# Kernel tuning notes

Hardware: AMD Instinct MI355X
Metric: run time of the kernel (lower is better)

Reference implementation:

```python
import jax, jax.numpy as jnp
import numpy as np

B, T, C, H = 2, 512, 1024, 16
D = C // H          # head dim 64
CS = 64             # chunk_size
NS_STEPS = 5
OMEGA_W = 8
KCONV = 4

# Polar Express per-iteration quintic coefficients (Amsel et al. 2025)
_PE_COEFFS = [
    (8.28721201814563, -23.595886519098837, 17.300387312530933),
    (4.107059111542203, -2.9478499167379106, 0.5448431082926601),
    (3.9486908534822946, -2.908902115962949, 0.5518191394370137),
    (3.3184196573706015, -2.488488024314874, 0.51004894012372),
    (2.300652019954817, -1.6689039845747493, 0.4188073119525673),
    (1.891301407787398, -1.2679958271945868, 0.37680408948524835),
    (1.8750014808534479, -1.2500016453999487, 0.3750001645474248),
    (1.875, -1.25, 0.375),
]

def _polar_express(X):
    # X: (..., D, D). Normalize to spectral-norm <= 1 via Frobenius bound, then iterate.
    nrm = jnp.sqrt(jnp.sum(X * X, axis=(-2, -1), keepdims=True)) + 1e-7
    Xn = X / (nrm * 1.01)
    for a, b, c in _PE_COEFFS[:NS_STEPS]:
        A = Xn @ jnp.swapaxes(Xn, -1, -2)
        Xn = a * Xn + (b * A + c * (A @ A)) @ Xn
    return Xn

def _polar_express_ste(X):
    # straight-through: forward = PE(X), backward = identity
    return X + jax.lax.stop_gradient(_polar_express(X) - X)

def _rms_norm(x):
    return x * jax.lax.rsqrt(jnp.mean(x * x, axis=-1, keepdims=True) + 1e-6)

def _poly_features(x):
    # phi(x) = sum_{i=1..p} x^i / i!  with poly_degree=2
    return x + 0.5 * x * x

def _short_conv(x, w, b):
    # causal depthwise conv; x:(B,T,C), w:(C,1,K), b:(C,)
    xc = jnp.transpose(x, (0, 2, 1))
    xc = jnp.pad(xc, ((0, 0), (0, 0), (KCONV - 1, 0)))
    y = jax.lax.conv_general_dilated(
        xc, w, window_strides=(1,), padding="VALID",
        dimension_numbers=("NCW", "OIW", "NCW"), feature_group_count=x.shape[-1])
    y = y + b[:, None]
    return jnp.transpose(y, (0, 2, 1))

def _linear_scan(h_init, gates, inputs):
    # h_t = g_t * h_{t-1} + in_t ; gates (B,cs,H), inputs (B,cs,H,D,D)
    g = gates[..., None, None]
    first = g[:, :1] * h_init[:, None] + inputs[:, :1]
    mod_in = jnp.concatenate([first, inputs[:, 1:]], axis=1)
    mod_g = jnp.concatenate([jnp.zeros_like(g[:, :1]), g[:, 1:]], axis=1)
    def comb(a, b):
        ga, xa = a; gb, xb = b
        return (ga * gb, gb * xa + xb)
    _, h_all = jax.lax.associative_scan(comb, (mod_g, mod_in), axis=1)
    return h_all, h_all[:, -1]

def _omega_aggregate(u, gamma):
    # sliding-window sum of gamma_i * u_i over last OMEGA_W positions, via cumsum
    cs = u.shape[1]
    cum = jnp.cumsum(gamma * u, axis=1)
    if OMEGA_W >= cs:
        return cum
    shifted = jnp.concatenate([jnp.zeros_like(cum[:, :OMEGA_W]), cum[:, :-OMEGA_W]], axis=1)
    return cum - shifted


def setup_inputs() -> dict:
    key = jax.random.key(0)
    ks = jax.random.split(key, 16)
    s = 0.02
    return {
        "x":   jax.random.normal(ks[0], (B, T, C), jnp.float32),
        "Wq":  jax.random.normal(ks[1], (C, C), jnp.float32) * s,
        "Wk":  jax.random.normal(ks[2], (C, C), jnp.float32) * s,
        "Wv":  jax.random.normal(ks[3], (C, C), jnp.float32) * s,
        "Wo":  jax.random.normal(ks[4], (C, C), jnp.float32) * s,
        "cqw": jax.random.normal(ks[5], (C, 1, KCONV), jnp.float32) * s,
        "cqb": jnp.zeros((C,), jnp.float32),
        "ckw": jax.random.normal(ks[6], (C, 1, KCONV), jnp.float32) * s,
        "ckb": jnp.zeros((C,), jnp.float32),
        "cvw": jax.random.normal(ks[7], (C, 1, KCONV), jnp.float32) * s,
        "cvb": jnp.zeros((C,), jnp.float32),
        "Wa":  jax.random.normal(ks[8], (H, C), jnp.float32) * s,
        "We":  jax.random.normal(ks[9], (H, C), jnp.float32) * s,
        "Wt":  jax.random.normal(ks[10], (H, C), jnp.float32) * s,
        "Wg":  jax.random.normal(ks[11], (H, C), jnp.float32) * s,
    }


def reference(x, Wq, Wk, Wv, Wo, cqw, cqb, ckw, ckb, cvw, cvb, Wa, We, Wt, Wg):
    Bsz, Tlen, Cdim = x.shape
    q = _short_conv(x @ Wq.T, cqw, cqb).reshape(Bsz, Tlen, H, D)
    k = _short_conv(x @ Wk.T, ckw, ckb).reshape(Bsz, Tlen, H, D)
    v = _short_conv(x @ Wv.T, cvw, cvb).reshape(Bsz, Tlen, H, D)
    q = _poly_features(_rms_norm(q))
    k = _poly_features(_rms_norm(k))
    alpha = jax.nn.sigmoid(x @ Wa.T)   # (B,T,H) memory retention gate
    eta   = jax.nn.sigmoid(x @ We.T)   # learning rate gate
    theta = jax.nn.sigmoid(x @ Wt.T)   # momentum gate
    gamma = jax.nn.sigmoid(x @ Wg.T)   # omega context gate

    nC = Tlen // CS
    def chunked(a):  # (B,T,...) -> (nC,B,CS,...)
        return jnp.moveaxis(a.reshape(Bsz, nC, CS, *a.shape[2:]), 1, 0)
    qc, kc, vc = chunked(q), chunked(k), chunked(v)
    ac, ec, tc, gc = chunked(alpha), chunked(eta), chunked(theta), chunked(gamma)

    M0 = jnp.zeros((Bsz, H, D, D), x.dtype)
    S0 = jnp.zeros((Bsz, H, D, D), x.dtype)

    def step(carry, inp):
        M, S = carry
        q_c, k_c, v_c, a_c, e_c, t_c, g_c = inp
        pred = jnp.einsum("bhvk,bchk->bchv", M, k_c)
        err = pred - v_c
        u = 2.0 * jnp.einsum("bchv,bchk->bchvk", err, k_c)     # per-token gradient
        u = _omega_aggregate(u, g_c[..., None, None])           # omega window
        mom_in = -(e_c[..., None, None] * u)
        chunk_S, S = _linear_scan(S, t_c, mom_in)               # momentum scan
        chunk_S_orth = _polar_express_ste(chunk_S)              # orthogonalize
        M_all, M = _linear_scan(M, a_c, chunk_S_orth)           # memory scan
        y_c = jnp.einsum("bchvk,bchk->bchv", M_all, q_c)        # read memory
        return (M, S), y_c

    _, ys = jax.lax.scan(step, (M0, S0), (qc, kc, vc, ac, ec, tc, gc))
    y = jnp.moveaxis(ys, 0, 1).reshape(Bsz, Tlen, H, D)
    y = _rms_norm(y).reshape(Bsz, Tlen, Cdim)
    return y @ Wo.T
```

## Files before the change

kernel.cpp:

```cpp
#include <hip/hip_runtime.h>

constexpr int Bsz = 2, Tsz = 512, Csz = 1024, Hsz = 16, Dsz = 64, CSz = 64;
constexpr int NCHUNK = 8, OW = 8;

typedef __attribute__((ext_vector_type(8))) _Float16 half8;
typedef __attribute__((ext_vector_type(4))) _Float16 half4;
typedef __attribute__((ext_vector_type(16))) float f32x16;

constexpr float INV_S = 1.0f / 2048.0f;

__device__ __forceinline__ void split_f16(float v, _Float16& hi, _Float16& lo) {
  _Float16 h = (_Float16)v;
  float r = v - (float)h;
  hi = h;
  lo = (_Float16)(r * 2048.0f);
}

#define MFMA2(accH, accL, ah, al, bh, bl)                                     \
  accH = __builtin_amdgcn_mfma_f32_32x32x16_f16(ah, bh, accH, 0, 0, 0);       \
  accL = __builtin_amdgcn_mfma_f32_32x32x16_f16(ah, bl, accL, 0, 0, 0);       \
  accL = __builtin_amdgcn_mfma_f32_32x32x16_f16(al, bh, accL, 0, 0, 0);

__global__ __launch_bounds__(256) void split_all_kernel(
    const float* __restrict__ x, const float* __restrict__ Wq,
    const float* __restrict__ Wk, const float* __restrict__ Wv,
    const float* __restrict__ Wo, const float* __restrict__ Wa,
    const float* __restrict__ We, const float* __restrict__ Wt,
    const float* __restrict__ Wg,
    _Float16* __restrict__ xh, _Float16* __restrict__ xl,
    _Float16* __restrict__ Wqh, _Float16* __restrict__ Wql,
    _Float16* __restrict__ Wkh, _Float16* __restrict__ Wkl,
    _Float16* __restrict__ Wvh, _Float16* __restrict__ Wvl,
    _Float16* __restrict__ Woh, _Float16* __restrict__ Wol,
    _Float16* __restrict__ gWh, _Float16* __restrict__ gWl) {
  const int y = blockIdx.y;
  const int tid = threadIdx.x;
  if (y < 5) {
    const float* src = (y == 0 ? x : y == 1 ? Wq : y == 2 ? Wk : y == 3 ? Wv : Wo);
    _Float16* dh = (y == 0 ? xh : y == 1 ? Wqh : y == 2 ? Wkh : y == 3 ? Wvh : Woh);
    _Float16* dl = (y == 0 ? xl : y == 1 ? Wql : y == 2 ? Wkl : y == 3 ? Wvl : Wol);
    size_t i = ((size_t)blockIdx.x * 256 + tid) * 4;
    float4 v = *(const float4*)(src + i);
    half4 h, l;
#pragma unroll
    for (int j = 0; j < 4; ++j) { _Float16 hh, ll; split_f16((&v.x)[j], hh, ll); h[j] = hh; l[j] = ll; }
    *(half4*)(dh + i) = h;
    *(half4*)(dl + i) = l;
  } else {
    if (blockIdx.x >= 64) return;
    size_t i = ((size_t)blockIdx.x * 256 + tid) * 4;
    int gsel = (int)(i >> 14);
    int off = (int)(i & 16383);
    const float* src = (gsel == 0 ? Wa : gsel == 1 ? We : gsel == 2 ? Wt : Wg);
    float4 v = *(const float4*)(src + off);
    half4 h, l;
#pragma unroll
    for (int j = 0; j < 4; ++j) { _Float16 hh, ll; split_f16((&v.x)[j], hh, ll); h[j] = hh; l[j] = ll; }
    *(half4*)(gWh + i) = h;
    *(half4*)(gWl + i) = l;
  }
}

__device__ __forceinline__ void gemm64_core(const _Float16* __restrict__ Agh,
                                            const _Float16* __restrict__ Agl,
                                            const _Float16* __restrict__ Bgh,
                                            const _Float16* __restrict__ Bgl,
                                            int m0, int n0, int tid, char* LB,
                                            f32x16& accH, f32x16& accL) {
  const int lane = tid & 63, wv = tid >> 6;
  const int mb = (wv >> 1) << 5, nb = (wv & 1) << 5;
  const int lr = tid >> 2;
  const int lch = (tid & 3) << 4;
  const int cb = lch << 1;
  const int wb0 = (lr << 7) + (cb ^ ((lr & 7) << 4));
  const int wb1 = (lr << 7) + ((cb + 16) ^ ((lr & 7) << 4));
  const _Float16* pah = Agh + (size_t)(m0 + lr) * Csz + lch;
  const _Float16* pal = Agl + (size_t)(m0 + lr) * Csz + lch;
  const _Float16* pbh = Bgh + (size_t)(n0 + lr) * Csz + lch;
  const _Float16* pbl = Bgl + (size_t)(n0 + lr) * Csz + lch;
  int ra_m[4], ra_n[4];
#pragma unroll
  for (int ks = 0; ks < 4; ++ks) {
    int rm = mb + (lane & 31), rn = nb + (lane & 31);
    int cB = (ks << 5) + ((lane >> 5) << 4);
    ra_m[ks] = (rm << 7) + (cB ^ ((rm & 7) << 4));
    ra_n[ks] = (rn << 7) + (cB ^ ((rn & 7) << 4));
  }
#pragma unroll
  for (int r = 0; r < 16; ++r) { accH[r] = 0.f; accL[r] = 0.f; }
  for (int k0 = 0; k0 < Csz; k0 += 64) {
    half8 vah0 = *(const half8*)(pah + k0), vah1 = *(const half8*)(pah + k0 + 8);
    half8 val0 = *(const half8*)(pal + k0), val1 = *(const half8*)(pal + k0 + 8);
    half8 vbh0 = *(const half8*)(pbh + k0), vbh1 = *(const half8*)(pbh + k0 + 8);
    half8 vbl0 = *(const half8*)(pbl + k0), vbl1 = *(const half8*)(pbl + k0 + 8);
    __syncthreads();
    *(half8*)(LB + wb0) = vah0;          *(half8*)(LB + wb1) = vah1;
    *(half8*)(LB + 8192 + wb0) = val0;   *(half8*)(LB + 8192 + wb1) = val1;
    *(half8*)(LB + 16384 + wb0) = vbh0;  *(half8*)(LB + 16384 + wb1) = vbh1;
    *(half8*)(LB + 24576 + wb0) = vbl0;  *(half8*)(LB + 24576 + wb1) = vbl1;
    __syncthreads();
    __builtin_amdgcn_s_setprio(1);
#pragma unroll
    for (int ks = 0; ks < 4; ++ks) {
      half8 ah = *(const half8*)(LB + ra_m[ks]);
      half8 al = *(const half8*)(LB + 8192 + ra_m[ks]);
      half8 bh = *(const half8*)(LB + 16384 + ra_n[ks]);
      half8 bl = *(const half8*)(LB + 24576 + ra_n[ks]);
      MFMA2(accH, accL, ah, al, bh, bl);
    }
    __builtin_amdgcn_s_setprio(0);
  }
}

__global__ __launch_bounds__(256) void qkvg_mfma(
    const _Float16* __restrict__ xh, const _Float16* __restrict__ xl,
    const _Float16* __restrict__ Wqh, const _Float16* __restrict__ Wql,
    const _Float16* __restrict__ Wkh, const _Float16* __restrict__ Wkl,
    const _Float16* __restrict__ Wvh, const _Float16* __restrict__ Wvl,
    const _Float16* __restrict__ gWh, const _Float16* __restrict__ gWl,
    float* __restrict__ qlin, float* __restrict__ klin, float* __restrict__ vlin,
    float* __restrict__ ga, float* __restrict__ ge,
    float* __restrict__ gt, float* __restrict__ gg) {
  __shared__ __attribute__((aligned(16))) char LB[32768];
  const int tid = threadIdx.x;
  const int by = blockIdx.y;
  const int m0 = blockIdx.x << 6;
  const _Float16 *Bh, *Bl;
  int n0;
  if (by < 48) {
    const int mat = by >> 4;
    n0 = (by & 15) << 6;
    Bh = (mat == 0 ? Wqh : mat == 1 ? Wkh : Wvh);
    Bl = (mat == 0 ? Wql : mat == 1 ? Wkl : Wvl);
  } else {
    n0 = 0;
    Bh = gWh;
    Bl = gWl;
  }
  f32x16 accH, accL;
  gemm64_core(xh, xl, Bh, Bl, m0, n0, tid, LB, accH, accL);
  const int lane = tid & 63, wv = tid >> 6;
  const int mb = (wv >> 1) << 5, nb = (wv & 1) << 5;
  const int crow = (lane >> 5) << 2, ccol = lane & 31;
  if (by < 48) {
    const int mat = by >> 4;
    float* O = (mat == 0 ? qlin : mat == 1 ? klin : vlin);
#pragma unroll
    for (int r = 0; r < 16; ++r) {
      int row = mb + crow + (r & 3) + ((r >> 2) << 3);
      O[(size_t)(m0 + row) * Csz + n0 + nb + ccol] = accH[r] + accL[r] * INV_S;
    }
  } else {
    const int col = nb + ccol;
    const int gsel = col >> 4, h = col & 15;
    float* outp = (gsel == 0 ? ga : gsel == 1 ? ge : gsel == 2 ? gt : gg);
#pragma unroll
    for (int r = 0; r < 16; ++r) {
      int row = mb + crow + (r & 3) + ((r >> 2) << 3);
      float v = accH[r] + accL[r] * INV_S;
      outp[(size_t)(m0 + row) * Hsz + h] = 1.f / (1.f + expf(-v));
    }
  }
}

__global__ __launch_bounds__(256) void out_mfma(
    const _Float16* __restrict__ yh, const _Float16* __restrict__ yl,
    const _Float16* __restrict__ Woh, const _Float16* __restrict__ Wol,
    float* __restrict__ out) {
  __shared__ __attribute__((aligned(16))) char LB[32768];
  const int tid = threadIdx.x;
  const int m0 = blockIdx.x << 6, n0 = blockIdx.y << 6;
  f32x16 accH, accL;
  gemm64_core(yh, yl, Woh, Wol, m0, n0, tid, LB, accH, accL);
  const int lane = tid & 63, wv = tid >> 6;
  const int mb = (wv >> 1) << 5, nb = (wv & 1) << 5;
  const int crow = (lane >> 5) << 2, ccol = lane & 31;
#pragma unroll
  for (int r = 0; r < 16; ++r) {
    int row = mb + crow + (r & 3) + ((r >> 2) << 3);
    out[(size_t)(m0 + row) * Csz + n0 + nb + ccol] = accH[r] + accL[r] * INV_S;
  }
}

__global__ __launch_bounds__(256) void conv3_kernel(const float* __restrict__ qlin,
                                                    const float* __restrict__ klin,
                                                    const float* __restrict__ vlin,
                                                    const float* __restrict__ cqw,
                                                    const float* __restrict__ ckw,
                                                    const float* __restrict__ cvw,
                                                    const float* __restrict__ cqb,
                                                    const float* __restrict__ ckb,
                                                    const float* __restrict__ cvb,
                                                    float* __restrict__ qp,
                                                    float* __restrict__ kp,
                                                    float* __restrict__ vp) {
  const int sel = blockIdx.y;
  const float* lin = (sel == 0 ? qlin : sel == 1 ? klin : vlin);
  const float* w = (sel == 0 ? cqw : sel == 1 ? ckw : cvw);
  const float* bias = (sel == 0 ? cqb : sel == 1 ? ckb : cvb);
  float* out = (sel == 0 ? qp : sel == 1 ? kp : vp);
  const int do_norm = (sel < 2);
  const int bt = blockIdx.x;
  const int b = bt >> 9, t = bt & 511;
  const int tid = threadIdx.x;
  const int c0 = tid << 2;
  float4 bv = *(const float4*)&bias[c0];
  float v0 = bv.x, v1 = bv.y, v2 = bv.z, v3 = bv.w;
  float4 w0 = *(const float4*)&w[(c0 + 0) * 4];
  float4 w1 = *(const float4*)&w[(c0 + 1) * 4];
  float4 w2 = *(const float4*)&w[(c0 + 2) * 4];
  float4 w3 = *(const float4*)&w[(c0 + 3) * 4];
  const float* base = lin + (size_t)b * Tsz * Csz + c0;
#pragma unroll
  for (int j = 0; j < 4; ++j) {
    int tt = t - 3 + j;
    if (tt < 0) continue;
    float4 xv = *(const float4*)(base + (size_t)tt * Csz);
    v0 += xv.x * (&w0.x)[j];
    v1 += xv.y * (&w1.x)[j];
    v2 += xv.z * (&w2.x)[j];
    v3 += xv.w * (&w3.x)[j];
  }
  if (do_norm) {
    float ss = v0 * v0 + v1 * v1 + v2 * v2 + v3 * v3;
    ss += __shfl_xor(ss, 1, 16);
    ss += __shfl_xor(ss, 2, 16);
    ss += __shfl_xor(ss, 4, 16);
    ss += __shfl_xor(ss, 8, 16);
    float scl = rsqrtf(ss * (1.f / 64.f) + 1e-6f);
    v0 *= scl; v1 *= scl; v2 *= scl; v3 *= scl;
    v0 += 0.5f * v0 * v0; v1 += 0.5f * v1 * v1; v2 += 0.5f * v2 * v2; v3 += 0.5f * v3 * v3;
  }
  float4 o = {v0, v1, v2, v3};
  *(float4*)(out + (size_t)bt * Csz + c0) = o;
}

__global__ __launch_bounds__(256) void rms_split_kernel(const float* __restrict__ in,
                                                        _Float16* __restrict__ yh,
                                                        _Float16* __restrict__ yl) {
  const int bt = blockIdx.x;
  const int tid = threadIdx.x;
  const int c0 = tid << 2;
  float4 xv = *(const float4*)(in + (size_t)bt * Csz + c0);
  float ss = xv.x * xv.x + xv.y * xv.y + xv.z * xv.z + xv.w * xv.w;
  ss += __shfl_xor(ss, 1, 16);
  ss += __shfl_xor(ss, 2, 16);
  ss += __shfl_xor(ss, 4, 16);
  ss += __shfl_xor(ss, 8, 16);
  float scl = rsqrtf(ss * (1.f / 64.f) + 1e-6f);
  half4 h, l;
#pragma unroll
  for (int j = 0; j < 4; ++j) {
    _Float16 hh, ll;
    split_f16((&xv.x)[j] * scl, hh, ll);
    h[j] = hh; l[j] = ll;
  }
  *(half4*)(yh + (size_t)bt * Csz + c0) = h;
  *(half4*)(yl + (size_t)bt * Csz + c0) = l;
}

__global__ __launch_bounds__(256) void mom_scan_kernel(const float* __restrict__ Mst,
                                                       const float* __restrict__ kp,
                                                       const float* __restrict__ vp,
                                                       const float* __restrict__ geta,
                                                       const float* __restrict__ gtheta,
                                                       const float* __restrict__ ggamma,
                                                       float* __restrict__ Sst,
                                                       float* __restrict__ chunkS, int ci) {
  __shared__ float Ml[4 * Dsz];
  __shared__ float errl[256];
  __shared__ float kkl[CSz * Dsz];
  __shared__ float gl[CSz], el[CSz], tl[CSz];
  const int blk = blockIdx.x;
  const int bh = blk >> 4, eb = blk & 15;
  const int b = bh >> 4, h = bh & 15;
  const int tid = threadIdx.x;
  Ml[tid & 255] = Mst[(size_t)bh * 4096 + eb * 4 * 64 + tid];
#pragma unroll
  for (int i = 0; i < 16; ++i) {
    int idx = i * 256 + tid;
    int t = idx >> 6, k = idx & 63;
    kkl[idx] = kp[(((size_t)b * Tsz + ci * CSz + t) * Hsz + h) * Dsz + k];
  }
  if (tid < CSz) {
    size_t gi = ((size_t)b * Tsz + ci * CSz + tid) * Hsz + h;
    gl[tid] = ggamma[gi];
    el[tid] = geta[gi];
    tl[tid] = gtheta[gi];
  }
  __syncthreads();
  {
    const int tt = tid >> 2, vl = tid & 3;
    float acc = 0.f;
#pragma unroll
    for (int i = 0; i < 16; ++i) {
      float4 m4 = *(const float4*)&Ml[vl * 64 + i * 4];
      float4 k4 = *(const float4*)&kkl[tt * 64 + i * 4];
      acc += m4.x * k4.x + m4.y * k4.y + m4.z * k4.z + m4.w * k4.w;
    }
    float vv = vp[(((size_t)b * Tsz + ci * CSz + tt) * Hsz + h) * Dsz + eb * 4 + vl];
    errl[tt * 4 + vl] = acc - vv;
  }
  __syncthreads();
  const int e = eb * 256 + tid;
  const int vloc = tid >> 6;
  const int k = tid & 63;
  float S = Sst[(size_t)bh * 4096 + e];
  float ring[OW];
  float wsum = 0.f;
  float* outp = chunkS + (size_t)bh * CSz * 4096 + e;
#pragma unroll
  for (int t = 0; t < CSz; ++t) {
    float u = 2.f * errl[t * 4 + vloc] * kkl[t * 64 + k];
    float val = gl[t] * u;
    wsum += val;
    if (t >= OW) wsum -= ring[t & (OW - 1)];
    ring[t & (OW - 1)] = val;
    S = tl[t] * S - el[t] * wsum;
    outp[(size_t)t * 4096] = S;
  }
  Sst[(size_t)bh * 4096 + e] = S;
}

__global__ __launch_bounds__(256) void fused_scan_kernel(float* __restrict__ chunkS,
                                                         const float* __restrict__ qp,
                                                         const float* __restrict__ kp,
                                                         const float* __restrict__ vp,
                                                         const float* __restrict__ galpha,
                                                         const float* __restrict__ geta,
                                                         const float* __restrict__ gtheta,
                                                         const float* __restrict__ ggamma,
                                                         float* __restrict__ Mst,
                                                         float* __restrict__ Sst,
                                                         float* __restrict__ ybuf,
                                                         int ci, int do_next) {
  __shared__ float buf[CSz * Dsz];
  __shared__ float al[CSz];
  __shared__ float Ml[4 * Dsz];
  __shared__ float errl[256];
  __shared__ float gl[CSz], el[CSz], tl[CSz];
  const int blk = blockIdx.x;
  const int bh = blk >> 4, eb = blk & 15;
  const int b = bh >> 4, h = bh & 15;
  const int tid = threadIdx.x;
  const int w = tid >> 6, lane = tid & 63;
  const int v = eb * 4 + w, k = lane;
  for (int i = tid; i < CSz * Dsz; i += 256) {
    int t = i >> 6, kk = i & 63;
    buf[i] = qp[(((size_t)b * Tsz + ci * CSz + t) * Hsz + h) * Dsz + kk];
  }
  if (tid < CSz) al[tid] = galpha[((size_t)b * Tsz + ci * CSz + tid) * Hsz + h];
  __syncthreads();
  float m = Mst[(size_t)bh * 4096 + v * 64 + k];
  const float* Xo = chunkS + (size_t)bh * CSz * 4096;
  for (int t = 0; t < CSz; ++t) {
    m = al[t] * m + Xo[(size_t)t * 4096 + v * 64 + k];
    float p = m * buf[t * 64 + k];
#pragma unroll
    for (int off = 32; off; off >>= 1) p += __shfl_xor(p, off, 64);
    if (lane == 0) ybuf[(((size_t)b * Tsz + ci * CSz + t) * Hsz + h) * Dsz + v] = p;
  }
  Mst[(size_t)bh * 4096 + v * 64 + k] = m;
  if (!do_next) return;
  Ml[w * 64 + k] = m;
  __syncthreads();
  const int cj = ci + 1;
#pragma unroll
  for (int i = 0; i < 16; ++i) {
    int idx = i * 256 + tid;
    int t = idx >> 6, kk = idx & 63;
    buf[idx] = kp[(((size_t)b * Tsz + cj * CSz + t) * Hsz + h) * Dsz + kk];
  }
  if (tid < CSz) {
    size_t gi = ((size_t)b * Tsz + cj * CSz + tid) * Hsz + h;
    gl[tid] = ggamma[gi];
    el[tid] = geta[gi];
    tl[tid] = gtheta[gi];
  }
  __syncthreads();
  {
    const int tt = tid >> 2, vl = tid & 3;
    float acc = 0.f;
#pragma unroll
    for (int i = 0; i < 16; ++i) {
      float4 m4 = *(const float4*)&Ml[vl * 64 + i * 4];
      float4 k4 = *(const float4*)&buf[tt * 64 + i * 4];
      acc += m4.x * k4.x + m4.y * k4.y + m4.z * k4.z + m4.w * k4.w;
    }
    float vv = vp[(((size_t)b * Tsz + cj * CSz + tt) * Hsz + h) * Dsz + eb * 4 + vl];
    errl[tt * 4 + vl] = acc - vv;
  }
  __syncthreads();
  const int e = eb * 256 + tid;
  const int vloc = tid >> 6;
  float S = Sst[(size_t)bh * 4096 + e];
  float ring[OW];
  float wsum = 0.f;
  float* outp = chunkS + (size_t)bh * CSz * 4096 + e;
#pragma unroll
  for (int t = 0; t < CSz; ++t) {
    float u = 2.f * errl[t * 4 + vloc] * buf[t * 64 + k];
    float val = gl[t] * u;
    wsum += val;
    if (t >= OW) wsum -= ring[t & (OW - 1)];
    ring[t & (OW - 1)] = val;
    S = tl[t] * S - el[t] * wsum;
    outp[(size_t)t * 4096] = S;
  }
  Sst[(size_t)bh * 4096 + e] = S;
}

__global__ __launch_bounds__(256, 3) void pe_mfma_kernel(float* __restrict__ chunkS) {
  __shared__ __attribute__((aligned(16))) _Float16 PL[6 * 4096];
  __shared__ float red[4];
  const int tid = threadIdx.x;
  const int lane = tid & 63;
  const int wv = tid >> 6;
  float* G = chunkS + (size_t)blockIdx.x * 4096;
  constexpr int PLO = 8192;
  constexpr int PT = 16384;
  char* const LB = (char*)PL;

  const int mb = (wv >> 1) << 5;
  const int nb = (wv & 1) << 5;
  const int crow = ((lane >> 5) << 2);
  const int ccol = lane & 31;

  int ra_m[4], ra_n[4];
#pragma unroll
  for (int ks = 0; ks < 4; ++ks) {
    int rm = mb + (lane & 31), rn = nb + (lane & 31);
    int cB = (ks << 5) + ((lane >> 5) << 4);
    ra_m[ks] = (rm << 7) + (cB ^ ((rm & 7) << 4));
    ra_n[ks] = (rn << 7) + (cB ^ ((rn & 7) << 4));
  }
  int sa[4];
  {
    const int base = (nb + ccol) << 7;
    const int sw = ((nb + ccol) & 7) << 4;
    const int c2 = crow << 1;
#pragma unroll
    for (int g = 0; g < 4; ++g) sa[g] = base + ((((mb + 8 * g) << 1) ^ sw) + c2);
  }
  int rowa[4];
#pragma unroll
  for (int j = 0; j < 4; ++j) {
    int rr = mb + crow + j;
    rowa[j] = (rr << 7) + (((nb + ccol) << 1) ^ ((rr & 7) << 4));
  }

#define LDF(PB, RA, ks) (*(const half8*)(LB + (PB) + (RA)[ks]))

  auto STS = [&](int PB, const _Float16* hs, const _Float16* ls) {
#pragma unroll
    for (int g = 0; g < 4; ++g) {
      half4 hv, lv;
#pragma unroll
      for (int j = 0; j < 4; ++j) { hv[j] = hs[g * 4 + j]; lv[j] = ls[g * 4 + j]; }
      *(half4*)(LB + PB + sa[g]) = hv;
      *(half4*)(LB + PB + PLO + sa[g]) = lv;
    }
  };
  auto STR = [&](int PB, const _Float16* hs, const _Float16* ls) {
#pragma unroll
    for (int r = 0; r < 16; ++r) {
      int off = rowa[r & 3] + ((r >> 2) << 10);
      *(_Float16*)(LB + PB + off) = hs[r];
      *(_Float16*)(LB + PB + PLO + off) = ls[r];
    }
  };

  float Xval[16];
  float ss = 0.f;
#pragma unroll
  for (int r = 0; r < 16; ++r) {
    int rr = mb + crow + (r & 3) + ((r >> 2) << 3);
    float xv = G[rr * 64 + nb + ccol];
    Xval[r] = xv;
    ss += xv * xv;
  }
#pragma unroll
  for (int off = 32; off; off >>= 1) ss += __shfl_xor(ss, off, 64);
  if (lane == 0) red[wv] = ss;
  __syncthreads();
  float tot = red[0] + red[1] + red[2] + red[3];
  float scale = 1.f / ((sqrtf(tot) + 1e-7f) * 1.01f);

  {
    _Float16 hs[16], ls[16];
#pragma unroll
    for (int r = 0; r < 16; ++r) {
      Xval[r] *= scale;
      split_f16(Xval[r], hs[r], ls[r]);
    }
    STR(0, hs, ls);
    STS(PT, hs, ls);
  }

  auto iter = [&](float ca, float cb, float cc, int PXB, int PAB, bool last) {
    __syncthreads();
    if (wv != 2) {
      f32x16 accH, accL;
#pragma unroll
      for (int r = 0; r < 16; ++r) { accH[r] = 0.f; accL[r] = 0.f; }
      __builtin_amdgcn_s_setprio(1);
#pragma unroll
      for (int ks = 0; ks < 4; ++ks) {
        half8 ah = LDF(PXB, ra_m, ks), al = LDF(PXB + PLO, ra_m, ks);
        half8 bh, bl;
        if (mb != nb) { bh = LDF(PXB, ra_n, ks); bl = LDF(PXB + PLO, ra_n, ks); }
        else { bh = ah; bl = al; }
        MFMA2(accH, accL, ah, al, bh, bl);
      }
      __builtin_amdgcn_s_setprio(0);
      _Float16 hs[16], ls[16];
#pragma unroll
      for (int r = 0; r < 16; ++r) split_f16(accH[r] + accL[r] * INV_S, hs[r], ls[r]);
      STS(PAB, hs, ls);
      if (wv == 1) STR(PAB, hs, ls);
    }
    __syncthreads();
    half8 fah[4], fal[4];
    f32x16 acWH, acWL;
#pragma unroll
    for (int r = 0; r < 16; ++r) { acWH[r] = 0.f; acWL[r] = 0.f; }
    __builtin_amdgcn_s_setprio(1);
#pragma unroll
    for (int ks = 0; ks < 4; ++ks) {
      fah[ks] = LDF(PAB, ra_m, ks);
      fal[ks] = LDF(PAB + PLO, ra_m, ks);
      half8 bh = LDF(PT, ra_n, ks), bl = LDF(PT + PLO, ra_n, ks);
      MFMA2(acWH, acWL, fah[ks], fal[ks], bh, bl);
    }
    __builtin_amdgcn_s_setprio(0);
    float Wval[16];
    {
      _Float16 hs[16], ls[16];
#pragma unroll
      for (int r = 0; r < 16; ++r) {
        Wval[r] = acWH[r] + acWL[r] * INV_S;
        split_f16(Wval[r], hs[r], ls[r]);
      }
      STS(PXB, hs, ls);
    }
    __syncthreads();
    f32x16 acUH, acUL;
#pragma unroll
    for (int r = 0; r < 16; ++r) { acUH[r] = 0.f; acUL[r] = 0.f; }
    __builtin_amdgcn_s_setprio(1);
#pragma unroll
    for (int ks = 0; ks < 4; ++ks) {
      half8 bh = LDF(PXB, ra_n, ks), bl = LDF(PXB + PLO, ra_n, ks);
      MFMA2(acUH, acUL, fah[ks], fal[ks], bh, bl);
    }
    __builtin_amdgcn_s_setprio(0);
    if (!last) {
      _Float16 hs[16], ls[16];
#pragma unroll
      for (int r = 0; r < 16; ++r) {
        float xn = ca * Xval[r] + cb * Wval[r] + cc * (acUH[r] + acUL[r] * INV_S);
        Xval[r] = xn;
        split_f16(xn, hs[r], ls[r]);
      }
      STR(PAB, hs, ls);
      STS(PT, hs, ls);
    } else {
#pragma unroll
      for (int r = 0; r < 16; ++r) {
        int rr = mb + crow + (r & 3) + ((r >> 2) << 3);
        G[rr * 64 + nb + ccol] = ca * Xval[r] + cb * Wval[r] + cc * (acUH[r] + acUL[r] * INV_S);
      }
    }
  };

  iter(8.28721201814563f, -23.595886519098837f, 17.300387312530933f, 0, 32768, false);
  iter(4.107059111542203f, -2.9478499167379106f, 0.5448431082926601f, 32768, 0, false);
  iter(3.9486908534822946f, -2.908902115962949f, 0.5518191394370137f, 0, 32768, false);
  iter(3.3184196573706015f, -2.488488024314874f, 0.51004894012372f, 32768, 0, false);
  iter(2.300652019954817f, -1.6689039845747493f, 0.4188073119525673f, 0, 32768, true);
}

extern "C" void kernel_launch(void* const* d_in, const int* in_sizes, int n_in,
                              void* d_out, int out_size, void* d_ws, size_t ws_size,
                              hipStream_t stream) {
  (void)in_sizes; (void)n_in; (void)out_size; (void)ws_size;
  const float* x   = (const float*)d_in[0];
  const float* Wq  = (const float*)d_in[1];
  const float* Wk  = (const float*)d_in[2];
  const float* Wv  = (const float*)d_in[3];
  const float* Wo  = (const float*)d_in[4];
  const float* cqw = (const float*)d_in[5];
  const float* cqb = (const float*)d_in[6];
  const float* ckw = (const float*)d_in[7];
  const float* ckb = (const float*)d_in[8];
  const float* cvw = (const float*)d_in[9];
  const float* cvb = (const float*)d_in[10];
  const float* Wa  = (const float*)d_in[11];
  const float* We  = (const float*)d_in[12];
  const float* Wt  = (const float*)d_in[13];
  const float* Wg  = (const float*)d_in[14];
  float* out = (float*)d_out;

  float* p = (float*)d_ws;
  const size_t NBTC = (size_t)Bsz * Tsz * Csz;
  const size_t NBTH = (size_t)Bsz * Tsz * Hsz;
  const size_t NMAT = (size_t)Bsz * Hsz * Dsz * Dsz;
  const size_t NWW = (size_t)Csz * Csz;
  float* qlin = p; p += NBTC;
  float* klin = p; p += NBTC;
  float* vlin = p; p += NBTC;
  float* qp   = p; p += NBTC;
  float* kp   = p; p += NBTC;
  float* vp   = p; p += NBTC;
  float* ga   = p; p += NBTH;
  float* ge   = p; p += NBTH;
  float* gt   = p; p += NBTH;
  float* gg   = p; p += NBTH;
  float* Mst  = p; p += NMAT;
  float* Sst  = p; p += NMAT;
  float* chS  = p; p += (size_t)Bsz * Hsz * CSz * Dsz * Dsz;
  float* ybuf = p; p += NBTC;
  _Float16* hp = (_Float16*)p;
  _Float16* xh  = hp; hp += NBTC;
  _Float16* xl  = hp; hp += NBTC;
  _Float16* Wqh = hp; hp += NWW;
  _Float16* Wql = hp; hp += NWW;
  _Float16* Wkh = hp; hp += NWW;
  _Float16* Wkl = hp; hp += NWW;
  _Float16* Wvh = hp; hp += NWW;
  _Float16* Wvl = hp; hp += NWW;
  _Float16* Woh = hp; hp += NWW;
  _Float16* Wol = hp; hp += NWW;
  _Float16* gWh = hp; hp += (size_t)64 * Csz;
  _Float16* gWl = hp; hp += (size_t)64 * Csz;
  _Float16* yh  = hp; hp += NBTC;
  _Float16* yl  = hp; hp += NBTC;

  hipMemsetAsync(Mst, 0, NMAT * sizeof(float), stream);
  hipMemsetAsync(Sst, 0, NMAT * sizeof(float), stream);

  split_all_kernel<<<dim3(1024, 6), 256, 0, stream>>>(
      x, Wq, Wk, Wv, Wo, Wa, We, Wt, Wg,
      xh, xl, Wqh, Wql, Wkh, Wkl, Wvh, Wvl, Woh, Wol, gWh, gWl);
  qkvg_mfma<<<dim3(16, 49), 256, 0, stream>>>(
      xh, xl, Wqh, Wql, Wkh, Wkl, Wvh, Wvl, gWh, gWl,
      qlin, klin, vlin, ga, ge, gt, gg);
  conv3_kernel<<<dim3(Bsz * Tsz, 3), 256, 0, stream>>>(qlin, klin, vlin, cqw, ckw, cvw,
                                                       cqb, ckb, cvb, qp, kp, vp);

  mom_scan_kernel<<<Bsz * Hsz * 16, 256, 0, stream>>>(Mst, kp, vp, ge, gt, gg, Sst, chS, 0);
  for (int ci = 0; ci < NCHUNK; ++ci) {
    pe_mfma_kernel<<<Bsz * Hsz * CSz, 256, 0, stream>>>(chS);
    fused_scan_kernel<<<Bsz * Hsz * 16, 256, 0, stream>>>(chS, qp, kp, vp, ga, ge, gt, gg,
                                                          Mst, Sst, ybuf, ci,
                                                          ci < NCHUNK - 1 ? 1 : 0);
  }

  rms_split_kernel<<<Bsz * Tsz, 256, 0, stream>>>(ybuf, yh, yl);
  out_mfma<<<dim3(16, 16), 256, 0, stream>>>(yh, yl, Woh, Wol, out);
}
```

Before: 1.010 ms.

## Remap blocks to XCD-local head groups and software-pipeline memory scan loads

Adds a block-index decode so that blocks working on the same (batch, head) land on the same XCD in the scan and polar-express kernels. The goal is to keep chunkS data in that XCD's L2 between kernels. The memory scan loop in fused_scan_kernel is unrolled by four, prefetches the next four chunkS rows while computing the current ones, and interleaves the four shuffle reductions to hide latency. The decode assumes round-robin dispatch of blocks across 8 XCDs, and the unrolled loop raises register pressure.

```diff
diff --git a/kernel.cpp b/kernel.cpp
--- a/kernel.cpp
+++ b/kernel.cpp
@@ -20,6 +20,11 @@
   accH = __builtin_amdgcn_mfma_f32_32x32x16_f16(ah, bh, accH, 0, 0, 0);       \
   accL = __builtin_amdgcn_mfma_f32_32x32x16_f16(ah, bl, accL, 0, 0, 0);       \
   accL = __builtin_amdgcn_mfma_f32_32x32x16_f16(al, bh, accL, 0, 0, 0);
+
+__device__ __forceinline__ void xcd_decode(int bid, int& bh, int& idx) {
+  bh = (((bid >> 3) & 3) << 3) + (bid & 7);
+  idx = bid >> 5;
+}
 
 __global__ __launch_bounds__(256) void split_all_kernel(
     const float* __restrict__ x, const float* __restrict__ Wq,
@@ -271,8 +276,8 @@
   __shared__ float errl[256];
   __shared__ float kkl[CSz * Dsz];
   __shared__ float gl[CSz], el[CSz], tl[CSz];
-  const int blk = blockIdx.x;
-  const int bh = blk >> 4, eb = blk & 15;
+  int bh, eb;
+  xcd_decode(blockIdx.x, bh, eb);
   const int b = bh >> 4, h = bh & 15;
   const int tid = threadIdx.x;
   Ml[tid & 255] = Mst[(size_t)bh * 4096 + eb * 4 * 64 + tid];
@@ -339,8 +344,8 @@
   __shared__ float Ml[4 * Dsz];
   __shared__ float errl[256];
   __shared__ float gl[CSz], el[CSz], tl[CSz];
-  const int blk = blockIdx.x;
-  const int bh = blk >> 4, eb = blk & 15;
+  int bh, eb;
+  xcd_decode(blockIdx.x, bh, eb);
   const int b = bh >> 4, h = bh & 15;
   const int tid = threadIdx.x;
   const int w = tid >> 6, lane = tid & 63;
@@ -352,13 +357,38 @@
   if (tid < CSz) al[tid] = galpha[((size_t)b * Tsz + ci * CSz + tid) * Hsz + h];
   __syncthreads();
   float m = Mst[(size_t)bh * 4096 + v * 64 + k];
-  const float* Xo = chunkS + (size_t)bh * CSz * 4096;
-  for (int t = 0; t < CSz; ++t) {
-    m = al[t] * m + Xo[(size_t)t * 4096 + v * 64 + k];
-    float p = m * buf[t * 64 + k];
-#pragma unroll
-    for (int off = 32; off; off >>= 1) p += __shfl_xor(p, off, 64);
-    if (lane == 0) ybuf[(((size_t)b * Tsz + ci * CSz + t) * Hsz + h) * Dsz + v] = p;
+  const float* Xp = chunkS + (size_t)bh * CSz * 4096 + v * 64 + k;
+  float* yb = ybuf + (((size_t)b * Tsz + ci * CSz) * Hsz + h) * Dsz + v;
+  float x0 = Xp[0], x1 = Xp[4096], x2 = Xp[8192], x3 = Xp[12288];
+  for (int t0 = 0; t0 < CSz; t0 += 4) {
+    float n0, n1, n2, n3;
+    if (t0 + 4 < CSz) {
+      const float* Xn = Xp + (size_t)(t0 + 4) * 4096;
+      n0 = Xn[0]; n1 = Xn[4096]; n2 = Xn[8192]; n3 = Xn[12288];
+    } else {
+      n0 = n1 = n2 = n3 = 0.f;
+    }
+    float m0 = al[t0] * m + x0;
+    float m1 = al[t0 + 1] * m0 + x1;
+    float m2 = al[t0 + 2] * m1 + x2;
+    float m3 = al[t0 + 3] * m2 + x3;
+    m = m3;
+    float p0 = m0 * buf[(t0 + 0) * 64 + k];
+    float p1 = m1 * buf[(t0 + 1) * 64 + k];
+    float p2 = m2 * buf[(t0 + 2) * 64 + k];
+    float p3 = m3 * buf[(t0 + 3) * 64 + k];
+#pragma unroll
+    for (int off = 32; off; off >>= 1) {
+      p0 += __shfl_xor(p0, off, 64);
+      p1 += __shfl_xor(p1, off, 64);
+      p2 += __shfl_xor(p2, off, 64);
+      p3 += __shfl_xor(p3, off, 64);
+    }
+    if (lane < 4) {
+      float pj = (lane == 0 ? p0 : lane == 1 ? p1 : lane == 2 ? p2 : p3);
+      yb[(size_t)(t0 + lane) * Hsz * Dsz] = pj;
+    }
+    x0 = n0; x1 = n1; x2 = n2; x3 = n3;
   }
   Mst[(size_t)bh * 4096 + v * 64 + k] = m;
   if (!do_next) return;
@@ -416,7 +446,9 @@
   const int tid = threadIdx.x;
   const int lane = tid & 63;
   const int wv = tid >> 6;
-  float* G = chunkS + (size_t)blockIdx.x * 4096;
+  int bh, tmat;
+  xcd_decode(blockIdx.x, bh, tmat);
+  float* G = chunkS + ((size_t)bh * CSz + tmat) * 4096;
   constexpr int PLO = 8192;
   constexpr int PT = 16384;
   char* const LB = (char*)PL;
```

Result: faster. 871.8 us (-13.7%).
